# Kernel optimization log

Hardware: AMD Instinct MI355X
Metric: run time of the kernel (lower is better)

## Reference

```python
import jax, jax.numpy as jnp
import numpy as np

B, C, L = 256, 512, 150
CI = C // 4            # channel_in = in_dim // 4 = 128
K = 150                # one_hot_cls_num (depthwise kernel over length)
POOL = 150             # MaxPool2d kernel (150, 1)
EPS = 1e-5             # BatchNorm eps


def setup_inputs() -> dict:
    key = jax.random.key(0)
    ks = jax.random.split(key, 8)
    n = lambda k, shape, s: jax.random.normal(k, shape, jnp.float32) * s
    return {
        "x":    jax.random.normal(ks[0], (B, C, L, 1), jnp.float32),
        "Wv":   n(ks[1], (CI, C), 0.06),   "bv": jnp.zeros((CI,), jnp.float32),
        "Wq":   n(ks[2], (CI, CI), 0.12),  "bq": jnp.zeros((CI,), jnp.float32),
        "Wk":   n(ks[3], (CI, CI), 0.12),  "bk": jnp.zeros((CI,), jnp.float32),
        "gamma": n(ks[4], (), 1.0),
        "Wd":   n(ks[5], (2 * CI, K), 0.1), "bd": jnp.zeros((2 * CI,), jnp.float32),
        "Wp":   n(ks[6], (2 * CI, 2 * CI), 0.08), "bp": jnp.zeros((2 * CI,), jnp.float32),
        "bn_g": jnp.ones((2 * CI,), jnp.float32),
        "bn_b": jnp.zeros((2 * CI,), jnp.float32),
    }


def reference(x, Wv, bv, Wq, bq, Wk, bk, gamma, Wd, bd, Wp, bp, bn_g, bn_b):
    xb = x[..., 0]                                             # [B, C, L] (trailing width==1)
    # 1x1 convs are per-position matmuls over the channel dim
    v = jnp.einsum('oc,bcl->bol', Wv, xb) + bv[:, None]        # [B, CI, L]
    q = jnp.einsum('oc,bcl->bol', Wq, v) + bq[:, None]         # [B, CI, L]
    k = jnp.einsum('oc,bcl->bol', Wk, v) + bk[:, None]         # [B, CI, L]
    # raw (unscaled) attention: energy = q^T k, softmax over keys
    energy = jnp.einsum('bci,bcj->bij', q, k)                  # [B, L, L]
    attn = jax.nn.softmax(energy, axis=-1)
    # x = bmm(v, attn^T): out[b,c,i] = sum_j v[b,c,j] * attn[b,i,j]
    att_out = jnp.einsum('bcj,bij->bci', v, attn)              # [B, CI, L]
    cat = jnp.concatenate([gamma * att_out, v], axis=1)        # [B, 2CI, L]
    # MaxPool2d kernel=(150,1), stride=(150,1) over length
    Lp = L // POOL
    y = cat[:, :, : Lp * POOL].reshape(B, 2 * CI, Lp, POOL).max(axis=-1)
    y = y.reshape(B, -1)                                       # [B, 2CI*Lp]
    # depthwise conv kernel (K,1), VALID padding, groups = 2CI
    dw = jax.lax.conv_general_dilated(
        cat[:, :, :, None],                                    # [B, 2CI, L, 1]
        Wd[:, None, :, None],                                  # [2CI, 1, K, 1]
        window_strides=(1, 1), padding='VALID',
        dimension_numbers=('NCHW', 'OIHW', 'NCHW'),
        feature_group_count=2 * CI,
    ) + bd[None, :, None, None]                                # [B, 2CI, L-K+1, 1]
    # pointwise 1x1 conv
    pw = jnp.einsum('oc,bchw->bohw', Wp, dw) + bp[None, :, None, None]
    # BatchNorm2d in training mode: per-channel batch stats (biased variance)
    mean = pw.mean(axis=(0, 2, 3))
    var = pw.var(axis=(0, 2, 3))
    xn = (pw - mean[None, :, None, None]) * jax.lax.rsqrt(var[None, :, None, None] + EPS)
    out = jax.nn.relu(xn * bn_g[None, :, None, None] + bn_b[None, :, None, None])
    return jnp.concatenate([out.reshape(B, -1), y], axis=1)    # [B, 2CI*(L-K+1) + 2CI*Lp]
```

## Files before the change

kernel.cpp:

```cpp
#include <hip/hip_runtime.h>


typedef float f32x4  __attribute__((ext_vector_type(4)));
typedef float f32x16 __attribute__((ext_vector_type(16)));
typedef short s16x8  __attribute__((ext_vector_type(8)));
typedef unsigned short BF;

union U8 { s16x8 v; BF u[8]; uint2 d[2]; };

__device__ __forceinline__ BF bfhi(float f) { return (BF)(__float_as_uint(f) >> 16); }
__device__ __forceinline__ float bff(BF h) { return __uint_as_float(((unsigned)h) << 16); }
__device__ __forceinline__ BF bflo(float f, BF hi) { return bfhi(f - bff(hi)); }
__device__ __forceinline__ BF bfrne(float f) {
    unsigned u = __float_as_uint(f);
    u += 0x7fffu + ((u >> 16) & 1u);
    return (BF)(u >> 16);
}
__device__ __forceinline__ s16x8 ld8l(const BF* p) {
    U8 t; t.d[0] = *(const uint2*)p; t.d[1] = *(const uint2*)(p + 4); return t.v;
}
__device__ __forceinline__ void st4(BF* p, BF a, BF b, BF c, BF d) {
    uint2 t; t.x = (unsigned)a | ((unsigned)b << 16);
    t.y = (unsigned)c | ((unsigned)d << 16);
    *(uint2*)p = t;
}
#define MFMA(a, b, c)   __builtin_amdgcn_mfma_f32_16x16x32_bf16(a, b, c, 0, 0, 0)
#define MFMA32(a, b, c) __builtin_amdgcn_mfma_f32_32x32x16_bf16(a, b, c, 0, 0, 0)

__global__ __launch_bounds__(256)
void prep_all(const float* __restrict__ Wv, const float* __restrict__ Wq,
              const float* __restrict__ Wk, const float* __restrict__ bq,
              BF* __restrict__ wvh, BF* __restrict__ wvl,
              BF* __restrict__ wqh, BF* __restrict__ wql,
              float* __restrict__ cvec)
{
    __shared__ float qs[128][33], ks_[128][33];
    const int blk = blockIdx.x, tid = threadIdx.x;
    if (blk < 64) {
        int i = blk * 1024 + tid * 4;
        float4 v = *(const float4*)(Wv + i);
        BF h0 = bfhi(v.x), h1 = bfhi(v.y), h2 = bfhi(v.z), h3 = bfhi(v.w);
        st4(&wvh[i], h0, h1, h2, h3);
        st4(&wvl[i], bflo(v.x,h0), bflo(v.y,h1), bflo(v.z,h2), bflo(v.w,h3));
    } else if (blk < 80) {
        int bi = blk - 64;
        int d1_0 = (bi >> 2) * 32, d2_0 = (bi & 3) * 32;
        for (int i = tid; i < 4096; i += 256) {
            int o = i >> 5, c = i & 31;
            qs[o][c]  = Wq[o * 128 + d1_0 + c];
            ks_[o][c] = Wk[o * 128 + d2_0 + c];
        }
        __syncthreads();
        #pragma unroll
        for (int j = 0; j < 4; ++j) {
            int idx = j * 256 + tid;
            int d1 = idx >> 5, d2 = idx & 31;
            float s = 0.f;
            #pragma unroll 8
            for (int o = 0; o < 128; ++o) s = fmaf(qs[o][d1], ks_[o][d2], s);
            BF h = bfhi(s);
            wqh[(d1_0 + d1) * 128 + d2_0 + d2] = h;
            wql[(d1_0 + d1) * 128 + d2_0 + d2] = bflo(s, h);
        }
    } else {
        if (tid < 128) {
            float s = 0.f;
            for (int o = 0; o < 128; ++o) s += bq[o] * Wk[o * 128 + tid];
            cvec[tid] = s;
        }
    }
}

__global__ __launch_bounds__(1024, 4)
void fused_attn(const float* __restrict__ x, const BF* __restrict__ wvh,
                const BF* __restrict__ wvl, const float* __restrict__ bv,
                const BF* __restrict__ wqh, const BF* __restrict__ wql,
                const float* __restrict__ cvec, const float* __restrict__ gammap,
                const float* __restrict__ Wd, float* __restrict__ dw,
                float* __restrict__ out)
{
    __shared__ char smem[150272];
    BF (*vh)[140] = (BF(*)[140])smem;
    BF (*vl)[140] = (BF(*)[140])(smem + 44800);
    BF (*xt)[2][160][36] = (BF(*)[2][160][36])(smem + 89600);
    BF (*ts)[2][192][36] = (BF(*)[2][192][36])(smem + 89600);
    BF (*P)[172] = (BF(*)[172])(smem + 44800);
    float* smax = (float*)(smem + 144896);
    float* ssum = smax + 480;
    float* svp  = ssum + 480;

    const int b = blockIdx.x;
    const float* xb = x + (long)b * 76800;
    const int tid = threadIdx.x;
    const int lane = tid & 63, w = tid >> 6;
    const int li = lane & 15, gq = lane >> 4;
    const float gamma = gammap[0];

    if (w < 8) {
        const int wm = w & 1, wn = w >> 1;
        f32x4 acc[5][2];
        #pragma unroll
        for (int mf = 0; mf < 5; ++mf)
            #pragma unroll
            for (int nf = 0; nf < 2; ++nf) acc[mf][nf] = f32x4{0.f,0.f,0.f,0.f};
        s16x8 bh[2], bl[2];
        #pragma unroll
        for (int nf = 0; nf < 2; ++nf) {
            long g = (long)(wn*32 + nf*16 + li)*512 + gq*8;
            bh[nf] = *(const s16x8*)(wvh + g);
            bl[nf] = *(const s16x8*)(wvl + g);
        }
        __syncthreads();
        for (int p = 0; p < 16; ++p) {
            s16x8 nbh[2], nbl[2];
            if (p < 15) {
                #pragma unroll
                for (int nf = 0; nf < 2; ++nf) {
                    long g = (long)(wn*32 + nf*16 + li)*512 + (p+1)*32 + gq*8;
                    nbh[nf] = *(const s16x8*)(wvh + g);
                    nbl[nf] = *(const s16x8*)(wvl + g);
                }
            }
            const BF (*xh)[36]  = xt[p & 1][0];
            const BF (*xl2)[36] = xt[p & 1][1];
            #pragma unroll
            for (int mf = 0; mf < 5; ++mf) {
                int row = wm*80 + mf*16 + li;
                s16x8 ah = ld8l(&xh[row][gq*8]);
                s16x8 al = ld8l(&xl2[row][gq*8]);
                #pragma unroll
                for (int nf = 0; nf < 2; ++nf) {
                    acc[mf][nf] = MFMA(al, bh[nf], acc[mf][nf]);
                    acc[mf][nf] = MFMA(ah, bl[nf], acc[mf][nf]);
                    acc[mf][nf] = MFMA(ah, bh[nf], acc[mf][nf]);
                }
            }
            if (p < 15) {
                #pragma unroll
                for (int nf = 0; nf < 2; ++nf) { bh[nf] = nbh[nf]; bl[nf] = nbl[nf]; }
            }
            __syncthreads();
        }
        #pragma unroll
        for (int nf = 0; nf < 2; ++nf) {
            int c = wn*32 + nf*16 + li;
            float bvv = bv[c];
            #pragma unroll
            for (int mf = 0; mf < 5; ++mf)
                #pragma unroll
                for (int r = 0; r < 4; ++r) {
                    int l = wm*80 + mf*16 + gq*4 + r;
                    float f = acc[mf][nf][r] + bvv;
                    BF h = bfhi(f);
                    vh[l][c] = h;
                    vl[l][c] = bflo(f, h);
                }
        }
    } else {
        const int sw = w - 8;
        float cur[3][4];
        auto ldchunk = [&](int p) {
            #pragma unroll
            for (int it = 0; it < 3; ++it) {
                int l = it*64 + lane;
                #pragma unroll
                for (int cc = 0; cc < 4; ++cc)
                    cur[it][cc] = (l < 150) ? xb[(p*32 + sw*4 + cc)*150 + l] : 0.f;
            }
        };
        auto wrchunk = [&](int buf) {
            #pragma unroll
            for (int it = 0; it < 3; ++it) {
                int l = it*64 + lane;
                if (l < 160) {
                    BF h0=bfhi(cur[it][0]), h1=bfhi(cur[it][1]);
                    BF h2=bfhi(cur[it][2]), h3=bfhi(cur[it][3]);
                    st4(&xt[buf][0][l][sw*4], h0, h1, h2, h3);
                    st4(&xt[buf][1][l][sw*4], bflo(cur[it][0],h0), bflo(cur[it][1],h1),
                                              bflo(cur[it][2],h2), bflo(cur[it][3],h3));
                }
            }
        };
        ldchunk(0); wrchunk(0); ldchunk(1);
        __syncthreads();
        for (int p = 0; p < 16; ++p) {
            if (p < 15) {
                wrchunk((p + 1) & 1);
                if (p < 14) ldchunk(p + 2);
            }
            __syncthreads();
        }
    }
    __syncthreads();

    f32x4 eacc[2][4];
    #pragma unroll
    for (int a = 0; a < 2; ++a)
        #pragma unroll
        for (int b2 = 0; b2 < 4; ++b2) eacc[a][b2] = f32x4{0.f,0.f,0.f,0.f};
    const int iw = w / 3, jw = w % 3;
    const int l31 = lane & 31, hi5 = lane >> 5;

    for (int pr = 0; pr < 2; ++pr) {
        if (w < 10) {
            const int s2 = w / 5, jt = w % 5;
            const int ss = pr*2 + s2;
            f32x16 tacc;
            #pragma unroll
            for (int r = 0; r < 16; ++r) tacc[r] = 0.f;
            const int cg2 = ss*32 + l31;
            const int jr0 = jt*32 + l31;
            #pragma unroll
            for (int kc = 0; kc < 8; ++kc) {
                int kof = kc*16 + hi5*8;
                s16x8 bh = *(const s16x8*)(wqh + (long)cg2*128 + kof);
                s16x8 bl = *(const s16x8*)(wql + (long)cg2*128 + kof);
                s16x8 ah = ld8l(&vh[jr0][kof]);
                s16x8 al = ld8l(&vl[jr0][kof]);
                tacc = MFMA32(al, bh, tacc);
                tacc = MFMA32(ah, bl, tacc);
                tacc = MFMA32(ah, bh, tacc);
            }
            #pragma unroll
            for (int r = 0; r < 16; ++r) {
                int j = jt*32 + (r & 3) + 8*(r >> 2) + 4*hi5;
                float f = tacc[r];
                BF h = bfhi(f);
                ts[s2][0][j][l31] = h;
                ts[s2][1][j][l31] = bflo(f, h);
            }
        } else if (pr == 0) {
            int t2 = tid - 640;
            int r = t2 >> 1, hf = t2 & 1;
            if (r < 160) {
                float s = 0.f;
                #pragma unroll 8
                for (int d2 = hf*64; d2 < hf*64 + 64; ++d2)
                    s += cvec[d2] * bff(vh[r][d2]);
                svp[hf*192 + r] = s;
            }
        }
        __syncthreads();
        if (w < 15) {
            #pragma unroll
            for (int s2 = 0; s2 < 2; ++s2) {
                int scol = (pr*2 + s2)*32 + gq*8;
                s16x8 ah[2], al[2];
                #pragma unroll
                for (int mf2 = 0; mf2 < 2; ++mf2) {
                    int row = iw*32 + mf2*16 + li;
                    ah[mf2] = ld8l(&vh[row][scol]);
                    al[mf2] = ld8l(&vl[row][scol]);
                }
                #pragma unroll
                for (int nf = 0; nf < 4; ++nf) {
                    int jr = jw*64 + nf*16 + li;
                    s16x8 bh = ld8l(&ts[s2][0][jr][gq*8]);
                    s16x8 bl = ld8l(&ts[s2][1][jr][gq*8]);
                    #pragma unroll
                    for (int mf2 = 0; mf2 < 2; ++mf2) {
                        eacc[mf2][nf] = MFMA(ah[mf2], bh, eacc[mf2][nf]);
                        eacc[mf2][nf] = MFMA(ah[mf2], bl, eacc[mf2][nf]);
                        eacc[mf2][nf] = MFMA(al[mf2], bh, eacc[mf2][nf]);
                    }
                }
            }
        }
        __syncthreads();
    }

    if (w < 15) {
        #pragma unroll
        for (int nf = 0; nf < 4; ++nf) {
            int j = jw*64 + nf*16 + li;
            float sv = svp[j] + svp[192 + j];
            #pragma unroll
            for (int mf2 = 0; mf2 < 2; ++mf2)
                #pragma unroll
                for (int r = 0; r < 4; ++r)
                    eacc[mf2][nf][r] += sv;
        }
        #pragma unroll
        for (int mf2 = 0; mf2 < 2; ++mf2)
            #pragma unroll
            for (int r = 0; r < 4; ++r) {
                int i = iw*32 + mf2*16 + gq*4 + r;
                float m = -3.4e38f;
                #pragma unroll
                for (int nf = 0; nf < 4; ++nf) {
                    int j = jw*64 + nf*16 + li;
                    if (j < 150) m = fmaxf(m, eacc[mf2][nf][r]);
                }
                #pragma unroll
                for (int o = 1; o < 16; o <<= 1) m = fmaxf(m, __shfl_xor(m, o));
                if (li == 0) smax[jw*160 + i] = m;
            }
    }
    __syncthreads();
    if (w < 15) {
        #pragma unroll
        for (int mf2 = 0; mf2 < 2; ++mf2)
            #pragma unroll
            for (int r = 0; r < 4; ++r) {
                int i = iw*32 + mf2*16 + gq*4 + r;
                float gm = fmaxf(fmaxf(smax[i], smax[160 + i]), smax[320 + i]);
                float rs_ = 0.f;
                #pragma unroll
                for (int nf = 0; nf < 4; ++nf) {
                    int j = jw*64 + nf*16 + li;
                    float e = (j < 150) ? __expf(eacc[mf2][nf][r] - gm) : 0.f;
                    eacc[mf2][nf][r] = e;
                    rs_ += e;
                }
                #pragma unroll
                for (int o = 1; o < 16; o <<= 1) rs_ += __shfl_xor(rs_, o);
                if (li == 0) ssum[jw*160 + i] = rs_;
            }
    }
    __syncthreads();
    if (w < 15) {
        #pragma unroll
        for (int mf2 = 0; mf2 < 2; ++mf2)
            #pragma unroll
            for (int r = 0; r < 4; ++r) {
                int i = iw*32 + mf2*16 + gq*4 + r;
                float inv = 1.f / (ssum[i] + ssum[160 + i] + ssum[320 + i]);
                #pragma unroll
                for (int nf = 0; nf < 4; ++nf) {
                    int j = jw*64 + nf*16 + li;
                    if (j < 160) P[i][j] = bfrne(eacc[mf2][nf][r] * inv);
                }
            }
    }
    __syncthreads();

    {
        const int pc = w & 7, pi = w >> 3;
        f32x4 oacc[5];
        #pragma unroll
        for (int i = 0; i < 5; ++i) oacc[i] = f32x4{0.f,0.f,0.f,0.f};
        #pragma unroll
        for (int ks = 0; ks < 5; ++ks) {
            int c = pc*16 + li;
            int j0 = ks*32 + gq*8;
            U8 t;
            #pragma unroll
            for (int e = 0; e < 8; ++e) t.u[e] = vh[j0 + e][c];
            #pragma unroll
            for (int nf2 = 0; nf2 < 5; ++nf2) {
                int ir = pi*80 + nf2*16 + li;
                s16x8 bp = ld8l(&P[ir][ks*32 + gq*8]);
                oacc[nf2] = MFMA(t.v, bp, oacc[nf2]);
            }
        }

        float* pmax = smax;
        float* pdot = ssum;
        #pragma unroll
        for (int r = 0; r < 4; ++r) {
            int c = pc*16 + gq*4 + r;
            float mx = -3.4e38f, dt = 0.f;
            #pragma unroll
            for (int nf2 = 0; nf2 < 5; ++nf2) {
                int l = pi*80 + nf2*16 + li;
                if (l < 150) {
                    float val = gamma * oacc[nf2][r];
                    mx = fmaxf(mx, val);
                    dt = fmaf(val, Wd[c*150 + l], dt);
                }
            }
            #pragma unroll
            for (int o = 1; o < 16; o <<= 1) {
                mx = fmaxf(mx, __shfl_xor(mx, o));
                dt += __shfl_xor(dt, o);
            }
            if (li == 0) { pmax[pi*128 + c] = mx; pdot[pi*128 + c] = dt; }
        }
        __syncthreads();
        if (tid < 128) {
            out[(long)b*512 + 256 + tid] = fmaxf(pmax[tid], pmax[128 + tid]);
            dw[b*256 + tid] = pdot[tid] + pdot[128 + tid];
        } else if (tid >= 256 && tid < 768) {
            int t2 = tid - 256, c2 = t2 >> 2, q3 = t2 & 3;
            int l0 = (q3*150) >> 2, l1 = ((q3 + 1)*150) >> 2;
            float mx = -3.4e38f, dt = 0.f;
            for (int l = l0; l < l1; ++l) {
                float val = bff(vh[l][c2]);
                mx = fmaxf(mx, val);
                dt = fmaf(val, Wd[(128 + c2)*150 + l], dt);
            }
            mx = fmaxf(mx, __shfl_xor(mx, 1));
            dt += __shfl_xor(dt, 1);
            mx = fmaxf(mx, __shfl_xor(mx, 2));
            dt += __shfl_xor(dt, 2);
            if (q3 == 0) {
                out[(long)b*512 + 256 + 128 + c2] = mx;
                dw[b*256 + 128 + c2] = dt;
            }
        }
    }
}

__global__ __launch_bounds__(256)
void tail_pwbn(const float* __restrict__ dw, const float* __restrict__ Wp,
               const float* __restrict__ bn_g, const float* __restrict__ bn_b,
               float* __restrict__ out)
{
    __shared__ float wp_s[256];
    __shared__ float rs[4], rs2[4];
    const int o = blockIdx.x, t = threadIdx.x;
    const int lane = t & 63, w = t >> 6;
    wp_s[t] = Wp[o * 256 + t];
    __syncthreads();
    const float4* dr = (const float4*)(dw + (long)t * 256);
    float acc = 0.f;
    #pragma unroll 8
    for (int i = 0; i < 64; ++i) {
        float4 d4 = dr[i];
        acc = fmaf(d4.x, wp_s[i*4+0], acc);
        acc = fmaf(d4.y, wp_s[i*4+1], acc);
        acc = fmaf(d4.z, wp_s[i*4+2], acc);
        acc = fmaf(d4.w, wp_s[i*4+3], acc);
    }
    float s = acc, s2 = acc * acc;
    #pragma unroll
    for (int d = 1; d < 64; d <<= 1) { s += __shfl_xor(s, d); s2 += __shfl_xor(s2, d); }
    if (lane == 0) { rs[w] = s; rs2[w] = s2; }
    __syncthreads();
    float S  = rs[0] + rs[1] + rs[2] + rs[3];
    float S2 = rs2[0] + rs2[1] + rs2[2] + rs2[3];
    float mean = S * (1.f/256.f);
    float var  = S2 * (1.f/256.f) - mean * mean;
    float sc = rsqrtf(var + 1e-5f) * bn_g[o];
    float sh = bn_b[o] - mean * sc;
    out[(long)t * 512 + o] = fmaxf(fmaf(acc, sc, sh), 0.f);
}

extern "C" void kernel_launch(void* const* d_in, const int* in_sizes, int n_in,
                              void* d_out, int out_size, void* d_ws, size_t ws_size,
                              hipStream_t stream)
{
    (void)in_sizes; (void)n_in; (void)out_size; (void)ws_size;
    const float* x    = (const float*)d_in[0];
    const float* Wv   = (const float*)d_in[1];
    const float* bv   = (const float*)d_in[2];
    const float* Wq   = (const float*)d_in[3];
    const float* bq   = (const float*)d_in[4];
    const float* Wk   = (const float*)d_in[5];
    const float* bk   = (const float*)d_in[6];  (void)bk;
    const float* gam  = (const float*)d_in[7];
    const float* Wd   = (const float*)d_in[8];
    const float* Wp   = (const float*)d_in[10];
    const float* bn_g = (const float*)d_in[12];
    const float* bn_b = (const float*)d_in[13];
    float* out = (float*)d_out;

    char* wsb = (char*)d_ws;
    BF* wvh  = (BF*)wsb;
    BF* wvl  = (BF*)(wsb + 131072);
    BF* wqh  = (BF*)(wsb + 262144);
    BF* wql  = (BF*)(wsb + 294912);
    float* cvec = (float*)(wsb + 327680);
    float* dw   = (float*)(wsb + 328192);

    prep_all<<<81, 256, 0, stream>>>(Wv, Wq, Wk, bq, wvh, wvl, wqh, wql, cvec);
    fused_attn<<<256, 1024, 0, stream>>>(x, wvh, wvl, bv, wqh, wql, cvec,
                                         gam, Wd, dw, out);
    tail_pwbn<<<256, 256, 0, stream>>>(dw, Wp, bn_g, bn_b, out);
}
```

Before: 88.51 us.

## Split fused attention kernel into V-projection and attention kernels via packed global V

The single fused kernel is split in two. The first computes the V projection across 512 blocks, each handling half of the sequence length for one batch. It writes V as packed hi/lo bf16 words to global memory, together with per-half max-pool and depthwise partials for the V channels. The second kernel reads V from global instead of LDS, which shrinks its shared memory and should allow better occupancy and parallelism; the cost is an extra round trip of about 20 MB of V through memory plus one more launch.

New measurement: 107.7 us. 21.7% more time.

```diff
diff --git a/kernel.cpp b/kernel.cpp
--- a/kernel.cpp
+++ b/kernel.cpp
@@ -6,7 +6,7 @@
 typedef short s16x8  __attribute__((ext_vector_type(8)));
 typedef unsigned short BF;
 
-union U8 { s16x8 v; BF u[8]; uint2 d[2]; };
+union U8 { s16x8 v; BF u[8]; uint2 d[2]; unsigned w[4]; };
 
 __device__ __forceinline__ BF bfhi(float f) { return (BF)(__float_as_uint(f) >> 16); }
 __device__ __forceinline__ float bff(BF h) { return __uint_as_float(((unsigned)h) << 16); }
@@ -23,6 +23,19 @@
     uint2 t; t.x = (unsigned)a | ((unsigned)b << 16);
     t.y = (unsigned)c | ((unsigned)d << 16);
     *(uint2*)p = t;
+}
+__device__ __forceinline__ void ldv8(const unsigned* p, s16x8& hi, s16x8& lo) {
+    unsigned u[8];
+    *(uint4*)&u[0] = *(const uint4*)p;
+    *(uint4*)&u[4] = *(const uint4*)(p + 4);
+    U8 H, L;
+    #pragma unroll
+    for (int e = 0; e < 4; ++e) {
+        unsigned a = u[2*e], b2 = u[2*e + 1];
+        H.w[e] = (a >> 16) | (b2 & 0xffff0000u);
+        L.w[e] = (a & 0xffffu) | (b2 << 16);
+    }
+    hi = H.v; lo = L.v;
 }
 #define MFMA(a, b, c)   __builtin_amdgcn_mfma_f32_16x16x32_bf16(a, b, c, 0, 0, 0)
 #define MFMA32(a, b, c) __builtin_amdgcn_mfma_f32_32x32x16_bf16(a, b, c, 0, 0, 0)
@@ -71,33 +84,22 @@
     }
 }
 
-__global__ __launch_bounds__(1024, 4)
-void fused_attn(const float* __restrict__ x, const BF* __restrict__ wvh,
-                const BF* __restrict__ wvl, const float* __restrict__ bv,
-                const BF* __restrict__ wqh, const BF* __restrict__ wql,
-                const float* __restrict__ cvec, const float* __restrict__ gammap,
-                const float* __restrict__ Wd, float* __restrict__ dw,
-                float* __restrict__ out)
+__global__ __launch_bounds__(512, 4)
+void k1_v(const float* __restrict__ x, const BF* __restrict__ wvh,
+          const BF* __restrict__ wvl, const float* __restrict__ bv,
+          const float* __restrict__ Wd,
+          unsigned* __restrict__ vp, float* __restrict__ vpm,
+          float* __restrict__ vpd)
 {
-    __shared__ char smem[150272];
-    BF (*vh)[140] = (BF(*)[140])smem;
-    BF (*vl)[140] = (BF(*)[140])(smem + 44800);
-    BF (*xt)[2][160][36] = (BF(*)[2][160][36])(smem + 89600);
-    BF (*ts)[2][192][36] = (BF(*)[2][192][36])(smem + 89600);
-    BF (*P)[172] = (BF(*)[172])(smem + 44800);
-    float* smax = (float*)(smem + 144896);
-    float* ssum = smax + 480;
-    float* svp  = ssum + 480;
-
-    const int b = blockIdx.x;
-    const float* xb = x + (long)b * 76800;
-    const int tid = threadIdx.x;
-    const int lane = tid & 63, w = tid >> 6;
+    __shared__ BF xt[2][2][80][36];
+    const int bx = blockIdx.x;
+    const int b = bx & 255, lh = bx >> 8;
+    const int l0 = lh * 80;
+    const float* xb = x + (long)b * 76800 + l0;
+    const int tid = threadIdx.x, lane = tid & 63, w = tid >> 6;
     const int li = lane & 15, gq = lane >> 4;
-    const float gamma = gammap[0];
-
-    if (w < 8) {
-        const int wm = w & 1, wn = w >> 1;
+
+    if (w < 4) {
         f32x4 acc[5][2];
         #pragma unroll
         for (int mf = 0; mf < 5; ++mf)
@@ -106,7 +108,7 @@
         s16x8 bh[2], bl[2];
         #pragma unroll
         for (int nf = 0; nf < 2; ++nf) {
-            long g = (long)(wn*32 + nf*16 + li)*512 + gq*8;
+            long g = (long)(w*32 + nf*16 + li)*512 + gq*8;
             bh[nf] = *(const s16x8*)(wvh + g);
             bl[nf] = *(const s16x8*)(wvl + g);
         }
@@ -116,18 +118,18 @@
             if (p < 15) {
                 #pragma unroll
                 for (int nf = 0; nf < 2; ++nf) {
-                    long g = (long)(wn*32 + nf*16 + li)*512 + (p+1)*32 + gq*8;
+                    long g = (long)(w*32 + nf*16 + li)*512 + (p+1)*32 + gq*8;
                     nbh[nf] = *(const s16x8*)(wvh + g);
                     nbl[nf] = *(const s16x8*)(wvl + g);
                 }
             }
-            const BF (*xh)[36]  = xt[p & 1][0];
-            const BF (*xl2)[36] = xt[p & 1][1];
+            const BF (*xh)[36] = xt[p & 1][0];
+            const BF (*xl)[36] = xt[p & 1][1];
             #pragma unroll
             for (int mf = 0; mf < 5; ++mf) {
-                int row = wm*80 + mf*16 + li;
+                int row = mf*16 + li;
                 s16x8 ah = ld8l(&xh[row][gq*8]);
-                s16x8 al = ld8l(&xl2[row][gq*8]);
+                s16x8 al = ld8l(&xl[row][gq*8]);
                 #pragma unroll
                 for (int nf = 0; nf < 2; ++nf) {
                     acc[mf][nf] = MFMA(al, bh[nf], acc[mf][nf]);
@@ -143,41 +145,58 @@
         }
         #pragma unroll
         for (int nf = 0; nf < 2; ++nf) {
-            int c = wn*32 + nf*16 + li;
+            int c = w*32 + nf*16 + li;
             float bvv = bv[c];
+            float mx = -3.4e38f, dt = 0.f;
             #pragma unroll
             for (int mf = 0; mf < 5; ++mf)
                 #pragma unroll
                 for (int r = 0; r < 4; ++r) {
-                    int l = wm*80 + mf*16 + gq*4 + r;
+                    int ll = mf*16 + gq*4 + r;
                     float f = acc[mf][nf][r] + bvv;
                     BF h = bfhi(f);
-                    vh[l][c] = h;
-                    vl[l][c] = bflo(f, h);
-                }
+                    BF lo2 = bflo(f, h);
+                    vp[((long)b*160 + l0 + ll)*128 + c] = ((unsigned)h << 16) | lo2;
+                    if (l0 + ll < 150) {
+                        mx = fmaxf(mx, f);
+                        dt = fmaf(f, Wd[(128 + c)*150 + l0 + ll], dt);
+                    }
+                }
+            mx = fmaxf(mx, __shfl_xor(mx, 16)); dt += __shfl_xor(dt, 16);
+            mx = fmaxf(mx, __shfl_xor(mx, 32)); dt += __shfl_xor(dt, 32);
+            if (gq == 0) {
+                vpm[((long)lh*256 + b)*128 + c] = mx;
+                vpd[((long)lh*256 + b)*128 + c] = dt;
+            }
         }
     } else {
-        const int sw = w - 8;
-        float cur[3][4];
+        const int sw = w - 4;
+        const int bound = (lh == 0) ? 16 : 6;
+        float cur[2][8];
         auto ldchunk = [&](int p) {
             #pragma unroll
-            for (int it = 0; it < 3; ++it) {
-                int l = it*64 + lane;
-                #pragma unroll
-                for (int cc = 0; cc < 4; ++cc)
-                    cur[it][cc] = (l < 150) ? xb[(p*32 + sw*4 + cc)*150 + l] : 0.f;
+            for (int cc = 0; cc < 8; ++cc) {
+                int ch = p*32 + sw*8 + cc;
+                cur[0][cc] = xb[ch*150 + lane];
+                cur[1][cc] = (lane < bound) ? xb[ch*150 + 64 + lane] : 0.f;
             }
         };
         auto wrchunk = [&](int buf) {
             #pragma unroll
-            for (int it = 0; it < 3; ++it) {
-                int l = it*64 + lane;
-                if (l < 160) {
-                    BF h0=bfhi(cur[it][0]), h1=bfhi(cur[it][1]);
-                    BF h2=bfhi(cur[it][2]), h3=bfhi(cur[it][3]);
-                    st4(&xt[buf][0][l][sw*4], h0, h1, h2, h3);
-                    st4(&xt[buf][1][l][sw*4], bflo(cur[it][0],h0), bflo(cur[it][1],h1),
-                                              bflo(cur[it][2],h2), bflo(cur[it][3],h3));
+            for (int g2 = 0; g2 < 2; ++g2) {
+                BF h0 = bfhi(cur[0][g2*4+0]), h1 = bfhi(cur[0][g2*4+1]);
+                BF h2 = bfhi(cur[0][g2*4+2]), h3 = bfhi(cur[0][g2*4+3]);
+                st4(&xt[buf][0][lane][sw*8 + g2*4], h0, h1, h2, h3);
+                st4(&xt[buf][1][lane][sw*8 + g2*4],
+                    bflo(cur[0][g2*4+0],h0), bflo(cur[0][g2*4+1],h1),
+                    bflo(cur[0][g2*4+2],h2), bflo(cur[0][g2*4+3],h3));
+                if (lane < 16) {
+                    BF k0 = bfhi(cur[1][g2*4+0]), k1 = bfhi(cur[1][g2*4+1]);
+                    BF k2 = bfhi(cur[1][g2*4+2]), k3 = bfhi(cur[1][g2*4+3]);
+                    st4(&xt[buf][0][64 + lane][sw*8 + g2*4], k0, k1, k2, k3);
+                    st4(&xt[buf][1][64 + lane][sw*8 + g2*4],
+                        bflo(cur[1][g2*4+0],k0), bflo(cur[1][g2*4+1],k1),
+                        bflo(cur[1][g2*4+2],k2), bflo(cur[1][g2*4+3],k3));
                 }
             }
         };
@@ -191,7 +210,30 @@
             __syncthreads();
         }
     }
-    __syncthreads();
+}
+
+__global__ __launch_bounds__(1024, 8)
+void k2_attn(const unsigned* __restrict__ vp,
+             const BF* __restrict__ wqh, const BF* __restrict__ wql,
+             const float* __restrict__ cvec, const float* __restrict__ gammap,
+             const float* __restrict__ Wd,
+             const float* __restrict__ vpm, const float* __restrict__ vpd,
+             float* __restrict__ dw, float* __restrict__ out)
+{
+    __shared__ char smem[60672];
+    BF (*ts)[2][192][36] = (BF(*)[2][192][36])smem;
+    BF (*P)[172] = (BF(*)[172])smem;
+    float* smax = (float*)(smem + 55296);
+    float* ssum = smax + 480;
+    float* svp  = ssum + 480;
+
+    const int b = blockIdx.x;
+    const unsigned* vb = vp + (long)b * 20480;
+    const int tid = threadIdx.x;
+    const int lane = tid & 63, w = tid >> 6;
+    const int li = lane & 15, gq = lane >> 4;
+    const int l31 = lane & 31, hi5 = lane >> 5;
+    const float gamma = gammap[0];
 
     f32x4 eacc[2][4];
     #pragma unroll
@@ -199,7 +241,6 @@
         #pragma unroll
         for (int b2 = 0; b2 < 4; ++b2) eacc[a][b2] = f32x4{0.f,0.f,0.f,0.f};
     const int iw = w / 3, jw = w % 3;
-    const int l31 = lane & 31, hi5 = lane >> 5;
 
     for (int pr = 0; pr < 2; ++pr) {
         if (w < 10) {
@@ -208,15 +249,15 @@
             f32x16 tacc;
             #pragma unroll
             for (int r = 0; r < 16; ++r) tacc[r] = 0.f;
-            const int cg2 = ss*32 + l31;
-            const int jr0 = jt*32 + l31;
+            const unsigned* arow = vb + (jt*32 + l31)*128;
+            const long brow = (long)(ss*32 + l31)*128;
             #pragma unroll
             for (int kc = 0; kc < 8; ++kc) {
                 int kof = kc*16 + hi5*8;
-                s16x8 bh = *(const s16x8*)(wqh + (long)cg2*128 + kof);
-                s16x8 bl = *(const s16x8*)(wql + (long)cg2*128 + kof);
-                s16x8 ah = ld8l(&vh[jr0][kof]);
-                s16x8 al = ld8l(&vl[jr0][kof]);
+                s16x8 bh = *(const s16x8*)(wqh + brow + kof);
+                s16x8 bl = *(const s16x8*)(wql + brow + kof);
+                s16x8 ah, al;
+                ldv8(arow + kof, ah, al);
                 tacc = MFMA32(al, bh, tacc);
                 tacc = MFMA32(ah, bl, tacc);
                 tacc = MFMA32(ah, bh, tacc);
@@ -231,12 +272,18 @@
             }
         } else if (pr == 0) {
             int t2 = tid - 640;
+            unsigned* tz = (unsigned*)smem;
+            for (int z = t2; z < 2304; z += 384) {
+                int sb = z / 576, rz = z % 576;
+                tz[(sb*192 + 160)*18 + rz] = 0u;
+            }
             int r = t2 >> 1, hf = t2 & 1;
             if (r < 160) {
+                const unsigned* vr = vb + r*128 + hf*64;
                 float s = 0.f;
                 #pragma unroll 8
-                for (int d2 = hf*64; d2 < hf*64 + 64; ++d2)
-                    s += cvec[d2] * bff(vh[r][d2]);
+                for (int d2 = 0; d2 < 64; ++d2)
+                    s += cvec[hf*64 + d2] * bff((BF)(vr[d2] >> 16));
                 svp[hf*192 + r] = s;
             }
         }
@@ -247,11 +294,8 @@
                 int scol = (pr*2 + s2)*32 + gq*8;
                 s16x8 ah[2], al[2];
                 #pragma unroll
-                for (int mf2 = 0; mf2 < 2; ++mf2) {
-                    int row = iw*32 + mf2*16 + li;
-                    ah[mf2] = ld8l(&vh[row][scol]);
-                    al[mf2] = ld8l(&vl[row][scol]);
-                }
+                for (int mf2 = 0; mf2 < 2; ++mf2)
+                    ldv8(vb + (iw*32 + mf2*16 + li)*128 + scol, ah[mf2], al[mf2]);
                 #pragma unroll
                 for (int nf = 0; nf < 4; ++nf) {
                     int jr = jw*64 + nf*16 + li;
@@ -345,7 +389,8 @@
             int j0 = ks*32 + gq*8;
             U8 t;
             #pragma unroll
-            for (int e = 0; e < 8; ++e) t.u[e] = vh[j0 + e][c];
+            for (int e = 0; e < 8; ++e)
+                t.u[e] = (BF)(vb[(j0 + e)*128 + c] >> 16);
             #pragma unroll
             for (int nf2 = 0; nf2 < 5; ++nf2) {
                 int ir = pi*80 + nf2*16 + li;
@@ -380,23 +425,12 @@
         if (tid < 128) {
             out[(long)b*512 + 256 + tid] = fmaxf(pmax[tid], pmax[128 + tid]);
             dw[b*256 + tid] = pdot[tid] + pdot[128 + tid];
-        } else if (tid >= 256 && tid < 768) {
-            int t2 = tid - 256, c2 = t2 >> 2, q3 = t2 & 3;
-            int l0 = (q3*150) >> 2, l1 = ((q3 + 1)*150) >> 2;
-            float mx = -3.4e38f, dt = 0.f;
-            for (int l = l0; l < l1; ++l) {
-                float val = bff(vh[l][c2]);
-                mx = fmaxf(mx, val);
-                dt = fmaf(val, Wd[(128 + c2)*150 + l], dt);
-            }
-            mx = fmaxf(mx, __shfl_xor(mx, 1));
-            dt += __shfl_xor(dt, 1);
-            mx = fmaxf(mx, __shfl_xor(mx, 2));
-            dt += __shfl_xor(dt, 2);
-            if (q3 == 0) {
-                out[(long)b*512 + 256 + 128 + c2] = mx;
-                dw[b*256 + 128 + c2] = dt;
-            }
+        } else if (tid < 256) {
+            int c2 = tid - 128;
+            float m0 = vpm[(long)b*128 + c2];
+            float m1 = vpm[(long)(256 + b)*128 + c2];
+            out[(long)b*512 + 384 + c2] = fmaxf(m0, m1);
+            dw[b*256 + 128 + c2] = vpd[(long)b*128 + c2] + vpd[(long)(256 + b)*128 + c2];
         }
     }
 }
@@ -456,15 +490,19 @@
     float* out = (float*)d_out;
 
     char* wsb = (char*)d_ws;
-    BF* wvh  = (BF*)wsb;
-    BF* wvl  = (BF*)(wsb + 131072);
-    BF* wqh  = (BF*)(wsb + 262144);
-    BF* wql  = (BF*)(wsb + 294912);
+    BF* wvh   = (BF*)wsb;
+    BF* wvl   = (BF*)(wsb + 131072);
+    BF* wqh   = (BF*)(wsb + 262144);
+    BF* wql   = (BF*)(wsb + 294912);
     float* cvec = (float*)(wsb + 327680);
-    float* dw   = (float*)(wsb + 328192);
+    unsigned* vpck = (unsigned*)(wsb + 328192);
+    float* vpm  = (float*)(wsb + 21299712);
+    float* vpd  = (float*)(wsb + 21561856);
+    float* dw   = (float*)wsb;
 
     prep_all<<<81, 256, 0, stream>>>(Wv, Wq, Wk, bq, wvh, wvl, wqh, wql, cvec);
-    fused_attn<<<256, 1024, 0, stream>>>(x, wvh, wvl, bv, wqh, wql, cvec,
-                                         gam, Wd, dw, out);
+    k1_v<<<512, 512, 0, stream>>>(x, wvh, wvl, bv, Wd, vpck, vpm, vpd);
+    k2_attn<<<256, 1024, 0, stream>>>(vpck, wqh, wql, cvec, gam, Wd, vpm, vpd,
+                                      dw, out);
     tail_pwbn<<<256, 256, 0, stream>>>(dw, Wp, bn_g, bn_b, out);
 }
```

## Fuse softmax passes with online rescale, pack hi/lo bf16 tiles, pad LDS rows

Applied to the files above, without the earlier changes.

The softmax now computes partial max and partial exp-sum per key slice in one pass, then merges them online with a rescale factor. This removes one block-wide barrier and one pass over the scores. The transposed-Q tile stores hi and lo bf16 halves packed into 32-bit words and unpacks them in registers. LDS rows are padded so operands can be loaded as 16-byte vectors. The change also adds s_setprio around the MFMA loops and folds the two-thread bias dot product into one thread per row, at the cost of more LDS and extra exp calls.

Result: no change. 88.85 us (+0.4%).

```diff
diff --git a/kernel.cpp b/kernel.cpp
--- a/kernel.cpp
+++ b/kernel.cpp
@@ -6,7 +6,7 @@
 typedef short s16x8  __attribute__((ext_vector_type(8)));
 typedef unsigned short BF;
 
-union U8 { s16x8 v; BF u[8]; uint2 d[2]; };
+union U8 { s16x8 v; BF u[8]; uint2 d[2]; unsigned w[4]; };
 
 __device__ __forceinline__ BF bfhi(float f) { return (BF)(__float_as_uint(f) >> 16); }
 __device__ __forceinline__ float bff(BF h) { return __uint_as_float(((unsigned)h) << 16); }
@@ -23,6 +23,23 @@
     uint2 t; t.x = (unsigned)a | ((unsigned)b << 16);
     t.y = (unsigned)c | ((unsigned)d << 16);
     *(uint2*)p = t;
+}
+__device__ __forceinline__ void ldv8(const unsigned* p, s16x8& hi, s16x8& lo) {
+    unsigned u[8];
+    *(uint4*)&u[0] = *(const uint4*)p;
+    *(uint4*)&u[4] = *(const uint4*)(p + 4);
+    U8 H, L;
+    #pragma unroll
+    for (int e = 0; e < 4; ++e) {
+        unsigned a = u[2*e], b2 = u[2*e + 1];
+        H.w[e] = (a >> 16) | (b2 & 0xffff0000u);
+        L.w[e] = (a & 0xffffu) | (b2 << 16);
+    }
+    hi = H.v; lo = L.v;
+}
+__device__ __forceinline__ unsigned packf(float f) {
+    BF h = bfhi(f);
+    return ((unsigned)h << 16) | (unsigned)bflo(f, h);
 }
 #define MFMA(a, b, c)   __builtin_amdgcn_mfma_f32_16x16x32_bf16(a, b, c, 0, 0, 0)
 #define MFMA32(a, b, c) __builtin_amdgcn_mfma_f32_32x32x16_bf16(a, b, c, 0, 0, 0)
@@ -79,15 +96,15 @@
                 const float* __restrict__ Wd, float* __restrict__ dw,
                 float* __restrict__ out)
 {
-    __shared__ char smem[150272];
+    __shared__ char smem[161792];
     BF (*vh)[140] = (BF(*)[140])smem;
     BF (*vl)[140] = (BF(*)[140])(smem + 44800);
-    BF (*xt)[2][160][36] = (BF(*)[2][160][36])(smem + 89600);
-    BF (*ts)[2][192][36] = (BF(*)[2][192][36])(smem + 89600);
-    BF (*P)[172] = (BF(*)[172])(smem + 44800);
-    float* smax = (float*)(smem + 144896);
-    float* ssum = smax + 480;
-    float* svp  = ssum + 480;
+    BF (*xt)[2][160][40] = (BF(*)[2][160][40])(smem + 89600);
+    unsigned (*ts32)[192][44] = (unsigned(*)[192][44])(smem + 89600);
+    BF (*P)[168] = (BF(*)[168])(smem + 44800);
+    float* mg   = (float*)(smem + 157184);
+    float* sg   = (float*)(smem + 159104);
+    float* svec = (float*)(smem + 161024);
 
     const int b = blockIdx.x;
     const float* xb = x + (long)b * 76800;
@@ -121,13 +138,14 @@
                     nbl[nf] = *(const s16x8*)(wvl + g);
                 }
             }
-            const BF (*xh)[36]  = xt[p & 1][0];
-            const BF (*xl2)[36] = xt[p & 1][1];
+            const BF (*xh)[40]  = xt[p & 1][0];
+            const BF (*xl2)[40] = xt[p & 1][1];
+            __builtin_amdgcn_s_setprio(1);
             #pragma unroll
             for (int mf = 0; mf < 5; ++mf) {
                 int row = wm*80 + mf*16 + li;
-                s16x8 ah = ld8l(&xh[row][gq*8]);
-                s16x8 al = ld8l(&xl2[row][gq*8]);
+                s16x8 ah = *(const s16x8*)&xh[row][gq*8];
+                s16x8 al = *(const s16x8*)&xl2[row][gq*8];
                 #pragma unroll
                 for (int nf = 0; nf < 2; ++nf) {
                     acc[mf][nf] = MFMA(al, bh[nf], acc[mf][nf]);
@@ -135,6 +153,7 @@
                     acc[mf][nf] = MFMA(ah, bh[nf], acc[mf][nf]);
                 }
             }
+            __builtin_amdgcn_s_setprio(0);
             if (p < 15) {
                 #pragma unroll
                 for (int nf = 0; nf < 2; ++nf) { bh[nf] = nbh[nf]; bl[nf] = nbl[nf]; }
@@ -210,6 +229,7 @@
             for (int r = 0; r < 16; ++r) tacc[r] = 0.f;
             const int cg2 = ss*32 + l31;
             const int jr0 = jt*32 + l31;
+            __builtin_amdgcn_s_setprio(1);
             #pragma unroll
             for (int kc = 0; kc < 8; ++kc) {
                 int kof = kc*16 + hi5*8;
@@ -221,23 +241,24 @@
                 tacc = MFMA32(ah, bl, tacc);
                 tacc = MFMA32(ah, bh, tacc);
             }
+            __builtin_amdgcn_s_setprio(0);
             #pragma unroll
             for (int r = 0; r < 16; ++r) {
                 int j = jt*32 + (r & 3) + 8*(r >> 2) + 4*hi5;
-                float f = tacc[r];
-                BF h = bfhi(f);
-                ts[s2][0][j][l31] = h;
-                ts[s2][1][j][l31] = bflo(f, h);
+                ts32[s2][j][l31] = packf(tacc[r]);
             }
         } else if (pr == 0) {
             int t2 = tid - 640;
-            int r = t2 >> 1, hf = t2 & 1;
-            if (r < 160) {
+            if (t2 < 160) {
                 float s = 0.f;
-                #pragma unroll 8
-                for (int d2 = hf*64; d2 < hf*64 + 64; ++d2)
-                    s += cvec[d2] * bff(vh[r][d2]);
-                svp[hf*192 + r] = s;
+                #pragma unroll
+                for (int k = 0; k < 16; ++k) {
+                    U8 t; t.v = ld8l(&vh[t2][k*8]);
+                    #pragma unroll
+                    for (int e = 0; e < 8; ++e)
+                        s = fmaf(bff(t.u[e]), cvec[k*8 + e], s);
+                }
+                svec[t2] = s;
             }
         }
         __syncthreads();
@@ -255,8 +276,8 @@
                 #pragma unroll
                 for (int nf = 0; nf < 4; ++nf) {
                     int jr = jw*64 + nf*16 + li;
-                    s16x8 bh = ld8l(&ts[s2][0][jr][gq*8]);
-                    s16x8 bl = ld8l(&ts[s2][1][jr][gq*8]);
+                    s16x8 bh, bl;
+                    ldv8(&ts32[s2][jr][gq*8], bh, bl);
                     #pragma unroll
                     for (int mf2 = 0; mf2 < 2; ++mf2) {
                         eacc[mf2][nf] = MFMA(ah[mf2], bh, eacc[mf2][nf]);
@@ -273,7 +294,7 @@
         #pragma unroll
         for (int nf = 0; nf < 4; ++nf) {
             int j = jw*64 + nf*16 + li;
-            float sv = svp[j] + svp[192 + j];
+            float sv = svec[j];
             #pragma unroll
             for (int mf2 = 0; mf2 < 2; ++mf2)
                 #pragma unroll
@@ -293,7 +314,17 @@
                 }
                 #pragma unroll
                 for (int o = 1; o < 16; o <<= 1) m = fmaxf(m, __shfl_xor(m, o));
-                if (li == 0) smax[jw*160 + i] = m;
+                float rs_ = 0.f;
+                #pragma unroll
+                for (int nf = 0; nf < 4; ++nf) {
+                    int j = jw*64 + nf*16 + li;
+                    float e = (j < 150) ? __expf(eacc[mf2][nf][r] - m) : 0.f;
+                    eacc[mf2][nf][r] = e;
+                    rs_ += e;
+                }
+                #pragma unroll
+                for (int o = 1; o < 16; o <<= 1) rs_ += __shfl_xor(rs_, o);
+                if (li == 0) { mg[jw*160 + i] = m; sg[jw*160 + i] = rs_; }
             }
     }
     __syncthreads();
@@ -303,32 +334,16 @@
             #pragma unroll
             for (int r = 0; r < 4; ++r) {
                 int i = iw*32 + mf2*16 + gq*4 + r;
-                float gm = fmaxf(fmaxf(smax[i], smax[160 + i]), smax[320 + i]);
-                float rs_ = 0.f;
+                float m0 = mg[i], m1 = mg[160 + i], m2 = mg[320 + i];
+                float M = fmaxf(fmaxf(m0, m1), m2);
+                float S = fmaf(sg[i], __expf(m0 - M),
+                          fmaf(sg[160 + i], __expf(m1 - M),
+                               sg[320 + i] * __expf(m2 - M)));
+                float scale = __expf(mg[jw*160 + i] - M) / S;
                 #pragma unroll
                 for (int nf = 0; nf < 4; ++nf) {
                     int j = jw*64 + nf*16 + li;
-                    float e = (j < 150) ? __expf(eacc[mf2][nf][r] - gm) : 0.f;
-                    eacc[mf2][nf][r] = e;
-                    rs_ += e;
-                }
-                #pragma unroll
-                for (int o = 1; o < 16; o <<= 1) rs_ += __shfl_xor(rs_, o);
-                if (li == 0) ssum[jw*160 + i] = rs_;
-            }
-    }
-    __syncthreads();
-    if (w < 15) {
-        #pragma unroll
-        for (int mf2 = 0; mf2 < 2; ++mf2)
-            #pragma unroll
-            for (int r = 0; r < 4; ++r) {
-                int i = iw*32 + mf2*16 + gq*4 + r;
-                float inv = 1.f / (ssum[i] + ssum[160 + i] + ssum[320 + i]);
-                #pragma unroll
-                for (int nf = 0; nf < 4; ++nf) {
-                    int j = jw*64 + nf*16 + li;
-                    if (j < 160) P[i][j] = bfrne(eacc[mf2][nf][r] * inv);
+                    if (j < 160) P[i][j] = bfrne(eacc[mf2][nf][r] * scale);
                 }
             }
     }
@@ -354,8 +369,8 @@
             }
         }
 
-        float* pmax = smax;
-        float* pdot = ssum;
+        float* pmax = mg;
+        float* pdot = sg;
         #pragma unroll
         for (int r = 0; r < 4; ++r) {
             int c = pc*16 + gq*4 + r;
```
